# Kernel optimization log

Hardware: AMD Instinct MI355X
Metric: run time of the kernel (lower is better)

The kernel has to match this reference:

```python
import jax, jax.numpy as jnp
import numpy as np

EPS = 1e-5
DIM = 1024
HEADS = 8
DIM_HEAD = 64
INNER = HEADS * DIM_HEAD  # 512


def layernorm(x, g, b):
    mu = jnp.mean(x, axis=-1, keepdims=True)
    var = jnp.var(x, axis=-1, keepdims=True)
    return (x - mu) * jax.lax.rsqrt(var + EPS) * g + b


def setup_inputs() -> dict:
    key = jax.random.key(0)
    ks = jax.random.split(key, 5)
    b, t, n, m = 4, 4, 2048, 64
    x = jax.random.normal(ks[0], (b, t, n, DIM), dtype=jnp.float32)
    latents = jax.random.normal(ks[1], (b, t, m, DIM), dtype=jnp.float32)
    Wq = jax.random.normal(ks[2], (DIM, INNER), dtype=jnp.float32) * (DIM ** -0.5)
    Wkv = jax.random.normal(ks[3], (DIM, 2 * INNER), dtype=jnp.float32) * (DIM ** -0.5)
    Wo = jax.random.normal(ks[4], (INNER, DIM), dtype=jnp.float32) * (INNER ** -0.5)
    return {
        "x": x, "latents": latents,
        "g_x": jnp.ones((DIM,), jnp.float32), "b_x": jnp.zeros((DIM,), jnp.float32),
        "g_l": jnp.ones((DIM,), jnp.float32), "b_l": jnp.zeros((DIM,), jnp.float32),
        "Wq": Wq, "Wkv": Wkv, "Wo": Wo,
    }


def reference(x, latents, g_x, b_x, g_l, b_l, Wq, Wkv, Wo):
    b, t, n, d = x.shape
    m = latents.shape[2]
    h, dh = HEADS, DIM_HEAD
    scale = dh ** -0.5

    xn = layernorm(x, g_x, b_x)              # (b,t,n,d)
    ln = layernorm(latents, g_l, b_l)        # (b,t,m,d)

    q = jnp.einsum('btmd,de->btme', ln, Wq)  # (b,t,m,inner)
    kv_in = jnp.concatenate([xn, ln], axis=-2)           # (b,t,n+m,d)
    kv = jnp.einsum('btjd,de->btje', kv_in, Wkv)         # (b,t,n+m,2*inner)
    k, v = jnp.split(kv, 2, axis=-1)

    q = q.reshape(b, t, m, h, dh) * scale
    k = k.reshape(b, t, n + m, h, dh)
    v = v.reshape(b, t, n + m, h, dh)

    sim = jnp.einsum('btihd,btjhd->bhtij', q, k)         # (b,h,t,m,n+m)
    sim = sim - jax.lax.stop_gradient(jnp.max(sim, axis=-1, keepdims=True))
    attn = jax.nn.softmax(sim, axis=-1)
    out = jnp.einsum('bhtij,btjhd->btihd', attn, v)      # (b,t,m,h,dh)
    out = out.reshape(b, t, m, h * dh)
    return jnp.einsum('btme,ed->btmd', out, Wo)          # (b,t,m,d)
```

## Files before the change

kernel.cpp:

```cpp
#include <hip/hip_runtime.h>
#include <cstdint>
#include <cstddef>

typedef __attribute__((ext_vector_type(8))) short short8;
typedef __attribute__((ext_vector_type(4))) short short4v;
typedef __attribute__((ext_vector_type(4))) float f32x4;

__device__ __forceinline__ short f2bf(float f) {
    union { float f; unsigned u; } c; c.f = f;
    unsigned r = c.u + 0x7fffu + ((c.u >> 16) & 1u);
    return (short)(r >> 16);
}

__device__ __forceinline__ void gl2lds16(const void* g, void* l) {
    __builtin_amdgcn_global_load_lds(
        (const __attribute__((address_space(1))) void*)g,
        (__attribute__((address_space(3))) void*)l, 16, 0, 0);
}

__global__ __launch_bounds__(256) void wconv(
    const float* __restrict__ S, short* __restrict__ D, int K, int N, float scale)
{
    __shared__ float t[32][33];
    const int kt = blockIdx.x * 32, nt = blockIdx.y * 32;
    const int x = threadIdx.x & 31, y4 = (threadIdx.x >> 5) * 4;
    for (int i = 0; i < 4; i++)
        t[y4 + i][x] = S[(size_t)(kt + y4 + i) * N + nt + x];
    __syncthreads();
    for (int i = 0; i < 4; i++)
        D[(size_t)(nt + y4 + i) * K + kt + x] = f2bf(t[x][y4 + i] * scale);
}

__global__ __launch_bounds__(256) void ln_kernel(
    const float* __restrict__ x, const float* __restrict__ lat,
    const float* __restrict__ gx, const float* __restrict__ bx,
    const float* __restrict__ gl, const float* __restrict__ bl,
    short* __restrict__ Aout, short* __restrict__ Lq)
{
    const int blk = blockIdx.x;
    const int tid = threadIdx.x;
    const float *src, *g, *b; size_t drow; short* dst2 = nullptr;
    if (blk < 32768) {
        int bt = blk >> 11, i = blk & 2047;
        src = x + (size_t)blk * 1024; g = gx; b = bx;
        drow = (size_t)bt * 2112 + i;
    } else {
        int idx = blk - 32768;
        int bt = idx >> 6, i = idx & 63;
        src = lat + (size_t)idx * 1024; g = gl; b = bl;
        drow = (size_t)bt * 2112 + 2048 + i;
        dst2 = Lq + (size_t)idx * 1024;
    }
    float4 v = ((const float4*)src)[tid];
    float s  = v.x + v.y + v.z + v.w;
    float s2 = v.x * v.x + v.y * v.y + v.z * v.z + v.w * v.w;
    for (int off = 32; off >= 1; off >>= 1) { s += __shfl_down(s, off); s2 += __shfl_down(s2, off); }
    __shared__ float red[8];
    const int wv = tid >> 6, ln_ = tid & 63;
    if (ln_ == 0) { red[wv] = s; red[4 + wv] = s2; }
    __syncthreads();
    s  = red[0] + red[1] + red[2] + red[3];
    s2 = red[4] + red[5] + red[6] + red[7];
    const float mu   = s * (1.f / 1024.f);
    const float var  = s2 * (1.f / 1024.f) - mu * mu;
    const float rstd = rsqrtf(var + 1e-5f);
    float4 gv = ((const float4*)g)[tid];
    float4 bv = ((const float4*)b)[tid];
    short4v o;
    o[0] = f2bf((v.x - mu) * rstd * gv.x + bv.x);
    o[1] = f2bf((v.y - mu) * rstd * gv.y + bv.y);
    o[2] = f2bf((v.z - mu) * rstd * gv.z + bv.z);
    o[3] = f2bf((v.w - mu) * rstd * gv.w + bv.w);
    *(short4v*)(Aout + drow * 1024 + tid * 4) = o;
    if (dst2) *(short4v*)(dst2 + tid * 4) = o;
}

template <typename OutT>
__global__ __launch_bounds__(256) void gemm_bt(
    const short* __restrict__ A, const short* __restrict__ Bt,
    OutT* __restrict__ C, int M, int N, int K)
{
    __shared__ short As[128 * 32];
    __shared__ short Bs[128 * 32];
    const int tid  = threadIdx.x;
    const int wave = tid >> 6, lane = tid & 63;
    const int col  = lane & 15, quad = lane >> 4;
    const int m0 = blockIdx.x * 128, n0 = blockIdx.y * 128;
    const int wm = (wave >> 1) * 64, wn = (wave & 1) * 64;
    const int sr = tid >> 2;
    const int sk = (tid & 3) * 8;

    f32x4 acc[4][4];
    for (int i = 0; i < 4; i++) for (int j = 0; j < 4; j++) acc[i][j] = f32x4{0.f, 0.f, 0.f, 0.f};

    const short* Ar0 = A  + (size_t)(m0 + sr)      * K + sk;
    const short* Ar1 = A  + (size_t)(m0 + sr + 64) * K + sk;
    const short* Br0 = Bt + (size_t)(n0 + sr)      * K + sk;
    const short* Br1 = Bt + (size_t)(n0 + sr + 64) * K + sk;
    short* lA0 = &As[sr * 32 + sk];
    short* lA1 = &As[(sr + 64) * 32 + sk];
    short* lB0 = &Bs[sr * 32 + sk];
    short* lB1 = &Bs[(sr + 64) * 32 + sk];

    for (int k0 = 0; k0 < K; k0 += 32) {
        __syncthreads();
        gl2lds16(Ar0 + k0, lA0);
        gl2lds16(Ar1 + k0, lA1);
        gl2lds16(Br0 + k0, lB0);
        gl2lds16(Br1 + k0, lB1);
        __syncthreads();
        short8 af[4], bf[4];
        for (int mt = 0; mt < 4; mt++) af[mt] = *(const short8*)&As[(wm + mt * 16 + col) * 32 + quad * 8];
        for (int nt = 0; nt < 4; nt++) bf[nt] = *(const short8*)&Bs[(wn + nt * 16 + col) * 32 + quad * 8];
        for (int mt = 0; mt < 4; mt++)
            for (int nt = 0; nt < 4; nt++)
                acc[mt][nt] = __builtin_amdgcn_mfma_f32_16x16x32_bf16(af[mt], bf[nt], acc[mt][nt], 0, 0, 0);
    }
    for (int mt = 0; mt < 4; mt++)
        for (int nt = 0; nt < 4; nt++)
            for (int r = 0; r < 4; r++) {
                int row = m0 + wm + mt * 16 + quad * 4 + r;
                int cc  = n0 + wn + nt * 16 + col;
                float v = acc[mt][nt][r];
                if constexpr (sizeof(OutT) == 2) C[(size_t)row * N + cc] = (OutT)f2bf(v);
                else                             C[(size_t)row * N + cc] = v;
            }
}

__global__ __launch_bounds__(256) void transpose_v(const short* __restrict__ KV, short* __restrict__ Vt)
{
    __shared__ short tile[64 * 68];
    const int bth = blockIdx.y, bt = bth >> 3, h = bth & 7;
    const int jt = blockIdx.x * 64;
    const int tid = threadIdx.x;
    for (int it = 0; it < 2; ++it) {
        int s = tid + it * 256;
        int j = s >> 3, dv = (s & 7) * 8;
        short8 v = *(const short8*)(KV + (size_t)(bt * 2112 + jt + j) * 1024 + 512 + h * 64 + dv);
        short4v lo = {v[0], v[1], v[2], v[3]}, hi = {v[4], v[5], v[6], v[7]};
        *(short4v*)&tile[j * 68 + dv]     = lo;
        *(short4v*)&tile[j * 68 + dv + 4] = hi;
    }
    __syncthreads();
    for (int it = 0; it < 2; ++it) {
        int s = tid + it * 256;
        int d = s >> 3, jv = (s & 7) * 8;
        short8 o;
        for (int jj = 0; jj < 8; jj++) o[jj] = tile[(jv + jj) * 68 + d];
        *(short8*)(Vt + (size_t)(bth * 64 + d) * 2112 + jt + jv) = o;
    }
}

__global__ __launch_bounds__(256) void attn_kernel(
    const short* __restrict__ Q,
    const short* __restrict__ KV,
    const short* __restrict__ Vt,
    float* __restrict__ Opart,
    float* __restrict__ Mp,
    float* __restrict__ Lp)
{
    __shared__ short p_lds[4][64 * 72];
    __shared__ float sm[4][64];
    __shared__ float sl[4][64];
    __shared__ float oacc[64 * 64];

    const int wg = blockIdx.x;
    const int ck = blockIdx.y;
    const int wgc = wg * 4 + ck;
    const int bt = wg >> 3, h = wg & 7;
    const int tid = threadIdx.x;
    const int wave = tid >> 6, lane = tid & 63;
    const int col = lane & 15, quad = lane >> 4;

    short8 qf[4][2];
    for (int mt = 0; mt < 4; mt++)
        for (int ks = 0; ks < 2; ks++)
            qf[mt][ks] = *(const short8*)(Q + (size_t)(bt * 64 + mt * 16 + col) * 512
                                            + h * 64 + ks * 32 + quad * 8);

    float m_run[4][4], l_run[4][4];
    f32x4 o_acc[4][4];
    for (int mt = 0; mt < 4; mt++)
        for (int r = 0; r < 4; r++) { m_run[mt][r] = -__builtin_inff(); l_run[mt][r] = 0.f; }
    for (int mt = 0; mt < 4; mt++)
        for (int dt = 0; dt < 4; dt++) o_acc[mt][dt] = f32x4{0.f, 0.f, 0.f, 0.f};

    short* pl = p_lds[wave];

    for (int jb = ck * 4 + wave; jb < 33; jb += 16) {
        f32x4 s[4][4];
        for (int mt = 0; mt < 4; mt++) for (int nt = 0; nt < 4; nt++) s[mt][nt] = f32x4{0.f, 0.f, 0.f, 0.f};
        for (int nt = 0; nt < 4; nt++) {
            const int j = jb * 64 + nt * 16 + col;
            const short* kp = KV + (size_t)(bt * 2112 + j) * 1024 + h * 64 + quad * 8;
            short8 k0 = *(const short8*)kp;
            short8 k1 = *(const short8*)(kp + 32);
            for (int mt = 0; mt < 4; mt++) {
                s[mt][nt] = __builtin_amdgcn_mfma_f32_16x16x32_bf16(qf[mt][0], k0, s[mt][nt], 0, 0, 0);
                s[mt][nt] = __builtin_amdgcn_mfma_f32_16x16x32_bf16(qf[mt][1], k1, s[mt][nt], 0, 0, 0);
            }
        }
        for (int mt = 0; mt < 4; mt++)
            for (int r = 0; r < 4; r++) {
                float mx = fmaxf(fmaxf(s[mt][0][r], s[mt][1][r]), fmaxf(s[mt][2][r], s[mt][3][r]));
                for (int off = 8; off >= 1; off >>= 1) mx = fmaxf(mx, __shfl_xor(mx, off));
                float mnew = fmaxf(m_run[mt][r], mx);
                float alpha = __expf(m_run[mt][r] - mnew);
                float rs = 0.f;
                for (int nt = 0; nt < 4; nt++) {
                    float p = __expf(s[mt][nt][r] - mnew);
                    s[mt][nt][r] = p;
                    rs += p;
                }
                for (int off = 8; off >= 1; off >>= 1) rs += __shfl_xor(rs, off);
                m_run[mt][r] = mnew;
                l_run[mt][r] = l_run[mt][r] * alpha + rs;
                for (int dt = 0; dt < 4; dt++) o_acc[mt][dt][r] *= alpha;
            }
        for (int mt = 0; mt < 4; mt++)
            for (int nt = 0; nt < 4; nt++)
                for (int r = 0; r < 4; r++)
                    pl[(mt * 16 + quad * 4 + r) * 72 + nt * 16 + col] = f2bf(s[mt][nt][r]);
        for (int ks = 0; ks < 2; ks++) {
            short8 vf[4];
            for (int dt = 0; dt < 4; dt++)
                vf[dt] = *(const short8*)(Vt + (size_t)(wg * 64 + dt * 16 + col) * 2112
                                             + jb * 64 + ks * 32 + quad * 8);
            for (int mt = 0; mt < 4; mt++) {
                short8 pf = *(const short8*)(pl + (mt * 16 + col) * 72 + ks * 32 + quad * 8);
                for (int dt = 0; dt < 4; dt++)
                    o_acc[mt][dt] = __builtin_amdgcn_mfma_f32_16x16x32_bf16(pf, vf[dt], o_acc[mt][dt], 0, 0, 0);
            }
        }
    }

    if (col == 0)
        for (int mt = 0; mt < 4; mt++)
            for (int r = 0; r < 4; r++) {
                int row = mt * 16 + quad * 4 + r;
                sm[wave][row] = m_run[mt][r];
                sl[wave][row] = l_run[mt][r];
            }
    __syncthreads();
    for (int mt = 0; mt < 4; mt++)
        for (int r = 0; r < 4; r++) {
            int row = mt * 16 + quad * 4 + r;
            float M = fmaxf(fmaxf(sm[0][row], sm[1][row]), fmaxf(sm[2][row], sm[3][row]));
            float L = sl[0][row] * __expf(sm[0][row] - M) + sl[1][row] * __expf(sm[1][row] - M)
                    + sl[2][row] * __expf(sm[2][row] - M) + sl[3][row] * __expf(sm[3][row] - M);
            if (wave == 0 && col == 0) { Mp[wgc * 64 + row] = M; Lp[wgc * 64 + row] = L; }
            float sc = __expf(m_run[mt][r] - M);
            for (int dt = 0; dt < 4; dt++) o_acc[mt][dt][r] *= sc;
        }
    for (int i = tid; i < 64 * 64; i += 256) oacc[i] = 0.f;
    __syncthreads();
    for (int w = 0; w < 4; w++) {
        if (wave == w)
            for (int mt = 0; mt < 4; mt++)
                for (int dt = 0; dt < 4; dt++)
                    for (int r = 0; r < 4; r++)
                        oacc[(mt * 16 + quad * 4 + r) * 64 + dt * 16 + col] += o_acc[mt][dt][r];
        __syncthreads();
    }
    for (int i = tid; i < 64 * 64; i += 256)
        Opart[(size_t)wgc * 4096 + i] = oacc[i];
}

__global__ __launch_bounds__(256) void attn_merge(
    const float* __restrict__ Opart, const float* __restrict__ Mp,
    const float* __restrict__ Lp, short* __restrict__ AttO)
{
    int idx = blockIdx.x * 256 + threadIdx.x;
    int wg = idx >> 12, rd = idx & 4095, row = rd >> 6, d = rd & 63;
    float M = -__builtin_inff();
    for (int c = 0; c < 4; c++) M = fmaxf(M, Mp[(wg * 4 + c) * 64 + row]);
    float L = 0.f, O = 0.f;
    for (int c = 0; c < 4; c++) {
        float e = __expf(Mp[(wg * 4 + c) * 64 + row] - M);
        L += e * Lp[(wg * 4 + c) * 64 + row];
        O += e * Opart[(size_t)(wg * 4 + c) * 4096 + rd];
    }
    int bt = wg >> 3, h = wg & 7;
    AttO[(size_t)(bt * 64 + row) * 512 + h * 64 + d] = f2bf(O / L);
}

extern "C" void kernel_launch(void* const* d_in, const int* in_sizes, int n_in,
                              void* d_out, int out_size, void* d_ws, size_t ws_size,
                              hipStream_t stream)
{
    const float* x   = (const float*)d_in[0];
    const float* lat = (const float*)d_in[1];
    const float* g_x = (const float*)d_in[2];
    const float* b_x = (const float*)d_in[3];
    const float* g_l = (const float*)d_in[4];
    const float* b_l = (const float*)d_in[5];
    const float* Wq  = (const float*)d_in[6];
    const float* Wkv = (const float*)d_in[7];
    const float* Wo  = (const float*)d_in[8];
    float* out = (float*)d_out;

    char* ws = (char*)d_ws;
    size_t off = 0;
    auto alloc = [&](size_t bytes) { char* p = ws + off; off += (bytes + 255) & ~(size_t)255; return p; };
    short* A_kvin = (short*)alloc(33792ull * 1024 * 2);
    short* Lq     = (short*)alloc(1024ull * 1024 * 2);
    short* WkvT   = (short*)alloc(1024ull * 1024 * 2);
    short* WqT    = (short*)alloc(512ull * 1024 * 2);
    short* WoT    = (short*)alloc(1024ull * 512 * 2);
    short* KVb    = (short*)alloc(33792ull * 1024 * 2);
    short* Qb     = (short*)alloc(1024ull * 512 * 2);
    short* AttO   = (short*)alloc(1024ull * 512 * 2);
    short* Vt    = A_kvin;
    char*  sc2   = (char*)A_kvin + 36ull * 1024 * 1024;
    float* Opart = (float*)sc2;
    float* Mp    = (float*)(sc2 + 8388608);
    float* Lp    = (float*)(sc2 + 8388608 + 131072);

    wconv<<<dim3(32, 32), 256, 0, stream>>>(Wkv, WkvT, 1024, 1024, 1.0f);
    wconv<<<dim3(32, 16), 256, 0, stream>>>(Wq,  WqT,  1024, 512,  0.125f);
    wconv<<<dim3(16, 32), 256, 0, stream>>>(Wo,  WoT,  512,  1024, 1.0f);
    ln_kernel<<<33792, 256, 0, stream>>>(x, lat, g_x, b_x, g_l, b_l, A_kvin, Lq);
    gemm_bt<short><<<dim3(264, 8), 256, 0, stream>>>(A_kvin, WkvT, KVb, 33792, 1024, 1024);
    gemm_bt<short><<<dim3(8, 4), 256, 0, stream>>>(Lq, WqT, Qb, 1024, 512, 1024);
    transpose_v<<<dim3(33, 128), 256, 0, stream>>>(KVb, Vt);
    attn_kernel<<<dim3(128, 4), 256, 0, stream>>>(Qb, KVb, Vt, Opart, Mp, Lp);
    attn_merge<<<2048, 256, 0, stream>>>(Opart, Mp, Lp, AttO);
    gemm_bt<float><<<dim3(8, 8), 256, 0, stream>>>(AttO, WoT, out, 1024, 1024, 512);
}
```

Measured before the change: 420.0 us.

## Use wave-per-row layernorm, N-major GEMM grid, split KV GEMM, 8-way attention split

The layernorm kernel now assigns one row per wave instead of one row per block, which drops the LDS reduction and the block barrier. The GEMM grid is swapped so blockIdx.x walks N tiles, letting consecutive blocks share the same A rows in cache. The large KV GEMM is split into two launches. Attention is split 8 ways over the key blocks instead of 4, with oacc aliased onto p_lds to save LDS and raise occupancy, at the cost of more partial outputs for the merge kernel to combine.

```diff
diff --git a/kernel.cpp b/kernel.cpp
--- a/kernel.cpp
+++ b/kernel.cpp
@@ -37,55 +37,54 @@
     const float* __restrict__ gl, const float* __restrict__ bl,
     short* __restrict__ Aout, short* __restrict__ Lq)
 {
-    const int blk = blockIdx.x;
-    const int tid = threadIdx.x;
+    const int wave = threadIdx.x >> 6, lane = threadIdx.x & 63;
+    const int r = blockIdx.x * 4 + wave;
     const float *src, *g, *b; size_t drow; short* dst2 = nullptr;
-    if (blk < 32768) {
-        int bt = blk >> 11, i = blk & 2047;
-        src = x + (size_t)blk * 1024; g = gx; b = bx;
+    if (r < 32768) {
+        int bt = r >> 11, i = r & 2047;
+        src = x + (size_t)r * 1024; g = gx; b = bx;
         drow = (size_t)bt * 2112 + i;
     } else {
-        int idx = blk - 32768;
+        int idx = r - 32768;
         int bt = idx >> 6, i = idx & 63;
         src = lat + (size_t)idx * 1024; g = gl; b = bl;
         drow = (size_t)bt * 2112 + 2048 + i;
         dst2 = Lq + (size_t)idx * 1024;
     }
-    float4 v = ((const float4*)src)[tid];
-    float s  = v.x + v.y + v.z + v.w;
-    float s2 = v.x * v.x + v.y * v.y + v.z * v.z + v.w * v.w;
-    for (int off = 32; off >= 1; off >>= 1) { s += __shfl_down(s, off); s2 += __shfl_down(s2, off); }
-    __shared__ float red[8];
-    const int wv = tid >> 6, ln_ = tid & 63;
-    if (ln_ == 0) { red[wv] = s; red[4 + wv] = s2; }
-    __syncthreads();
-    s  = red[0] + red[1] + red[2] + red[3];
-    s2 = red[4] + red[5] + red[6] + red[7];
+    float4 v[4];
+    for (int j = 0; j < 4; j++) v[j] = ((const float4*)src)[lane + 64 * j];
+    float s = 0.f, s2 = 0.f;
+    for (int j = 0; j < 4; j++) {
+        s  += v[j].x + v[j].y + v[j].z + v[j].w;
+        s2 += v[j].x * v[j].x + v[j].y * v[j].y + v[j].z * v[j].z + v[j].w * v[j].w;
+    }
+    for (int off = 32; off >= 1; off >>= 1) { s += __shfl_xor(s, off); s2 += __shfl_xor(s2, off); }
     const float mu   = s * (1.f / 1024.f);
-    const float var  = s2 * (1.f / 1024.f) - mu * mu;
-    const float rstd = rsqrtf(var + 1e-5f);
-    float4 gv = ((const float4*)g)[tid];
-    float4 bv = ((const float4*)b)[tid];
-    short4v o;
-    o[0] = f2bf((v.x - mu) * rstd * gv.x + bv.x);
-    o[1] = f2bf((v.y - mu) * rstd * gv.y + bv.y);
-    o[2] = f2bf((v.z - mu) * rstd * gv.z + bv.z);
-    o[3] = f2bf((v.w - mu) * rstd * gv.w + bv.w);
-    *(short4v*)(Aout + drow * 1024 + tid * 4) = o;
-    if (dst2) *(short4v*)(dst2 + tid * 4) = o;
+    const float rstd = rsqrtf(s2 * (1.f / 1024.f) - mu * mu + 1e-5f);
+    for (int j = 0; j < 4; j++) {
+        float4 gv = ((const float4*)g)[lane + 64 * j];
+        float4 bv = ((const float4*)b)[lane + 64 * j];
+        short4v o;
+        o[0] = f2bf((v[j].x - mu) * rstd * gv.x + bv.x);
+        o[1] = f2bf((v[j].y - mu) * rstd * gv.y + bv.y);
+        o[2] = f2bf((v[j].z - mu) * rstd * gv.z + bv.z);
+        o[3] = f2bf((v[j].w - mu) * rstd * gv.w + bv.w);
+        *(short4v*)(Aout + drow * 1024 + (size_t)(lane + 64 * j) * 4) = o;
+        if (dst2) *(short4v*)(dst2 + (size_t)(lane + 64 * j) * 4) = o;
+    }
 }
 
 template <typename OutT>
 __global__ __launch_bounds__(256) void gemm_bt(
     const short* __restrict__ A, const short* __restrict__ Bt,
-    OutT* __restrict__ C, int M, int N, int K)
+    OutT* __restrict__ C, int N, int K)
 {
     __shared__ short As[128 * 32];
     __shared__ short Bs[128 * 32];
     const int tid  = threadIdx.x;
     const int wave = tid >> 6, lane = tid & 63;
     const int col  = lane & 15, quad = lane >> 4;
-    const int m0 = blockIdx.x * 128, n0 = blockIdx.y * 128;
+    const int n0 = blockIdx.x * 128, m0 = blockIdx.y * 128;
     const int wm = (wave >> 1) * 64, wn = (wave & 1) * 64;
     const int sr = tid >> 2;
     const int sk = (tid & 3) * 8;
@@ -159,14 +158,14 @@
     float* __restrict__ Mp,
     float* __restrict__ Lp)
 {
-    __shared__ short p_lds[4][64 * 72];
+    __shared__ __align__(16) short p_lds[4][64 * 72];
     __shared__ float sm[4][64];
     __shared__ float sl[4][64];
-    __shared__ float oacc[64 * 64];
+    float* oacc = (float*)&p_lds[0][0];
 
     const int wg = blockIdx.x;
     const int ck = blockIdx.y;
-    const int wgc = wg * 4 + ck;
+    const int wgc = wg * 8 + ck;
     const int bt = wg >> 3, h = wg & 7;
     const int tid = threadIdx.x;
     const int wave = tid >> 6, lane = tid & 63;
@@ -187,7 +186,7 @@
 
     short* pl = p_lds[wave];
 
-    for (int jb = ck * 4 + wave; jb < 33; jb += 16) {
+    for (int jb = ck * 4 + wave; jb < 33; jb += 32) {
         f32x4 s[4][4];
         for (int mt = 0; mt < 4; mt++) for (int nt = 0; nt < 4; nt++) s[mt][nt] = f32x4{0.f, 0.f, 0.f, 0.f};
         for (int nt = 0; nt < 4; nt++) {
@@ -273,12 +272,12 @@
     int idx = blockIdx.x * 256 + threadIdx.x;
     int wg = idx >> 12, rd = idx & 4095, row = rd >> 6, d = rd & 63;
     float M = -__builtin_inff();
-    for (int c = 0; c < 4; c++) M = fmaxf(M, Mp[(wg * 4 + c) * 64 + row]);
+    for (int c = 0; c < 8; c++) M = fmaxf(M, Mp[(wg * 8 + c) * 64 + row]);
     float L = 0.f, O = 0.f;
-    for (int c = 0; c < 4; c++) {
-        float e = __expf(Mp[(wg * 4 + c) * 64 + row] - M);
-        L += e * Lp[(wg * 4 + c) * 64 + row];
-        O += e * Opart[(size_t)(wg * 4 + c) * 4096 + rd];
+    for (int c = 0; c < 8; c++) {
+        float e = __expf(Mp[(wg * 8 + c) * 64 + row] - M);
+        L += e * Lp[(wg * 8 + c) * 64 + row];
+        O += e * Opart[(size_t)(wg * 8 + c) * 4096 + rd];
     }
     int bt = wg >> 3, h = wg & 7;
     AttO[(size_t)(bt * 64 + row) * 512 + h * 64 + d] = f2bf(O / L);
@@ -313,17 +312,19 @@
     short* Vt    = A_kvin;
     char*  sc2   = (char*)A_kvin + 36ull * 1024 * 1024;
     float* Opart = (float*)sc2;
-    float* Mp    = (float*)(sc2 + 8388608);
-    float* Lp    = (float*)(sc2 + 8388608 + 131072);
+    float* Mp    = (float*)(sc2 + 16777216);
+    float* Lp    = (float*)(sc2 + 16777216 + 262144);
 
     wconv<<<dim3(32, 32), 256, 0, stream>>>(Wkv, WkvT, 1024, 1024, 1.0f);
     wconv<<<dim3(32, 16), 256, 0, stream>>>(Wq,  WqT,  1024, 512,  0.125f);
     wconv<<<dim3(16, 32), 256, 0, stream>>>(Wo,  WoT,  512,  1024, 1.0f);
-    ln_kernel<<<33792, 256, 0, stream>>>(x, lat, g_x, b_x, g_l, b_l, A_kvin, Lq);
-    gemm_bt<short><<<dim3(264, 8), 256, 0, stream>>>(A_kvin, WkvT, KVb, 33792, 1024, 1024);
-    gemm_bt<short><<<dim3(8, 4), 256, 0, stream>>>(Lq, WqT, Qb, 1024, 512, 1024);
+    ln_kernel<<<8448, 256, 0, stream>>>(x, lat, g_x, b_x, g_l, b_l, A_kvin, Lq);
+    gemm_bt<short><<<dim3(8, 132), 256, 0, stream>>>(A_kvin, WkvT, KVb, 1024, 1024);
+    gemm_bt<short><<<dim3(8, 132), 256, 0, stream>>>(A_kvin + 16896ull * 1024, WkvT,
+                                                     KVb + 16896ull * 1024, 1024, 1024);
+    gemm_bt<short><<<dim3(4, 8), 256, 0, stream>>>(Lq, WqT, Qb, 512, 1024);
     transpose_v<<<dim3(33, 128), 256, 0, stream>>>(KVb, Vt);
-    attn_kernel<<<dim3(128, 4), 256, 0, stream>>>(Qb, KVb, Vt, Opart, Mp, Lp);
+    attn_kernel<<<dim3(128, 8), 256, 0, stream>>>(Qb, KVb, Vt, Opart, Mp, Lp);
     attn_merge<<<2048, 256, 0, stream>>>(Opart, Mp, Lp, AttO);
-    gemm_bt<float><<<dim3(8, 8), 256, 0, stream>>>(AttO, WoT, out, 1024, 1024, 512);
-}
+    gemm_bt<float><<<dim3(8, 8), 256, 0, stream>>>(AttO, WoT, out, 1024, 512);
+}
```

Result: slower. 456.9 us (+8.8%).
